# Kernel tuning notes

Hardware: AMD Instinct MI355X
Metric: run time of the kernel (lower is better)

## Reference

```python
import jax, jax.numpy as jnp
import numpy as np

TOP_K = 2  # config.num_experts_per_tok


def quick_gelu(x):
    return x * jax.nn.sigmoid(1.702 * x)


def setup_inputs() -> dict:
    key = jax.random.key(0)
    ks = jax.random.split(key, 6)
    B, S, H, I, E = 8, 4096, 512, 1024, 8
    s_h = 1.0 / np.sqrt(H).astype(np.float32)
    s_i = 1.0 / np.sqrt(I).astype(np.float32)
    return {
        "hidden_states": jax.random.normal(ks[0], (B, S, H), jnp.float32),
        "router_w": jax.random.normal(ks[1], (H, E), jnp.float32) * s_h,
        "router_b": jnp.zeros((E,), jnp.float32),
        "gate_up_proj": jax.random.normal(ks[2], (E, H, 2 * I), jnp.float32) * s_h,
        "gate_up_proj_bias": jnp.zeros((E, 2 * I), jnp.float32),
        "down_proj": jax.random.normal(ks[3], (E, I, H), jnp.float32) * s_i,
        "down_proj_bias": jnp.zeros((E, H), jnp.float32),
    }


def reference(hidden_states, router_w, router_b, gate_up_proj,
              gate_up_proj_bias, down_proj, down_proj_bias):
    B, S, H = hidden_states.shape
    E = router_b.shape[0]
    x = hidden_states.reshape(-1, H)          # [T, H]
    T = x.shape[0]

    # Router: top-k logits then softmax over the selected k
    logits = x @ router_w + router_b          # [T, E]
    top_w, sel = jax.lax.top_k(logits, TOP_K)  # [T, k]
    top_w = jax.nn.softmax(top_w, axis=-1)

    # Per-token per-expert combine weight (0 for unselected experts) [T, E]
    tok_w = jnp.zeros((T, E), x.dtype).at[jnp.arange(T)[:, None], sel].add(top_w)

    # Loop over the (small, fixed) expert axis; zero weights kill non-routed
    # tokens' contributions, matching the masked gather/scatter exactly.
    def body(acc, params):
        Wgu, bgu, Wd, bd, w_e = params        # w_e: [T]
        gu = x @ Wgu + bgu                    # [T, 2I]
        gate, up = jnp.split(gu, 2, axis=-1)
        act = (up + 1.0) * quick_gelu(gate)   # [T, I]
        out = act @ Wd + bd                   # [T, H]
        return acc + out * w_e[:, None], None

    acc0 = jnp.zeros((T, H), x.dtype)
    acc, _ = jax.lax.scan(
        body, acc0,
        (gate_up_proj, gate_up_proj_bias, down_proj, down_proj_bias, tok_w.T))
    return acc.reshape(B, S, H)
```

## Files before the change

### kernel.cpp

```cpp
#include <hip/hip_runtime.h>

#define T_TOK 32768
#define HDIM  512
#define IDIM  1024
#define NEXP  8
#define BM    64
#define KI    128

typedef float    f32x4 __attribute__((ext_vector_type(4)));
typedef _Float16 f16x8 __attribute__((ext_vector_type(8)));
typedef _Float16 f16x4 __attribute__((ext_vector_type(4)));

#define GL2LDS(gp, lp)                                                        \
    __builtin_amdgcn_global_load_lds(                                         \
        (const __attribute__((address_space(1))) void*)(gp),                  \
        (__attribute__((address_space(3))) void*)(lp), 16, 0, 0)

__global__ __launch_bounds__(256) void router_kernel(
    const float* __restrict__ x, const float* __restrict__ rw,
    const float* __restrict__ rb, int* __restrict__ cnt,
    int* __restrict__ btok, float* __restrict__ bw)
{
    __shared__ float Wl[HDIM * NEXP];
    __shared__ float xc[64 * 133];
    __shared__ float part[4 * 64 * 8];
    __shared__ int   bcnt[NEXP];
    __shared__ int   sbase[NEXP];

    const int tid = threadIdx.x;
    const int t0  = blockIdx.x * 64;

    if (tid < NEXP) bcnt[tid] = 0;

    for (int j = tid; j < HDIM * NEXP / 4; j += 256)
        ((float4*)Wl)[j] = ((const float4*)rw)[j];

    const int tl = tid & 63;
    const int q  = tid >> 6;

    float acc[8];
#pragma unroll
    for (int e = 0; e < 8; ++e) acc[e] = 0.f;

    for (int hc = 0; hc < 4; ++hc) {
        __syncthreads();
        for (int j = tid; j < 64 * 128 / 4; j += 256) {
            int row = j >> 5;
            int col = (j & 31) * 4;
            float4 v = *(const float4*)(x + (size_t)(t0 + row) * HDIM + hc * 128 + col);
            float* d = &xc[row * 133 + col];
            d[0] = v.x; d[1] = v.y; d[2] = v.z; d[3] = v.w;
        }
        __syncthreads();
#pragma unroll
        for (int hh = 0; hh < 32; ++hh) {
            int h = q * 32 + hh;
            float xv = xc[tl * 133 + h];
            const float* wrow = &Wl[(hc * 128 + h) * 8];
#pragma unroll
            for (int e = 0; e < 8; ++e) acc[e] += xv * wrow[e];
        }
    }
#pragma unroll
    for (int e = 0; e < 8; ++e) part[(q * 64 + tl) * 8 + e] = acc[e];
    __syncthreads();

    int e0 = 0, e1 = 0, l0 = 0, l1 = 0;
    float w0 = 0.f, w1 = 0.f;
    if (tid < 64) {
        float lg[8];
#pragma unroll
        for (int e = 0; e < 8; ++e)
            lg[e] = part[(0 * 64 + tid) * 8 + e] + part[(1 * 64 + tid) * 8 + e] +
                    part[(2 * 64 + tid) * 8 + e] + part[(3 * 64 + tid) * 8 + e] + rb[e];
#pragma unroll
        for (int e = 1; e < 8; ++e) if (lg[e] > lg[e0]) e0 = e;
        e1 = (e0 == 0) ? 1 : 0;
#pragma unroll
        for (int e = 0; e < 8; ++e) if (e != e0 && lg[e] > lg[e1]) e1 = e;
        float z = __expf(lg[e1] - lg[e0]);
        w0 = 1.f / (1.f + z);
        w1 = z * w0;
        l0 = atomicAdd(&bcnt[e0], 1);
        l1 = atomicAdd(&bcnt[e1], 1);
    }
    __syncthreads();
    if (tid < NEXP) sbase[tid] = atomicAdd(&cnt[tid], bcnt[tid]);
    __syncthreads();
    if (tid < 64) {
        int t  = t0 + tid;
        int s0 = sbase[e0] + l0;
        btok[e0 * T_TOK + s0] = t;  bw[e0 * T_TOK + s0] = w0;
        int s1 = sbase[e1] + l1;
        btok[e1 * T_TOK + s1] = t;  bw[e1 * T_TOK + s1] = w1;
    }
}

template <int R, int C>
__global__ __launch_bounds__(256) void transpose_cvt(
    const float* __restrict__ src, _Float16* __restrict__ dst)
{
    __shared__ float tile[32][33];
    const int e  = blockIdx.z;
    const int rb = blockIdx.y * 32, cb = blockIdx.x * 32;
    const int t  = threadIdx.x;
    {
        const int lr = t >> 3, lc = (t & 7) * 4;
        float4 v = *(const float4*)(src + ((size_t)e * R + rb + lr) * C + cb + lc);
        tile[lr][lc + 0] = v.x; tile[lr][lc + 1] = v.y;
        tile[lr][lc + 2] = v.z; tile[lr][lc + 3] = v.w;
    }
    __syncthreads();
    {
        const int c = t >> 3, r4 = (t & 7) * 4;
        f16x4 h;
        h[0] = (_Float16)tile[r4 + 0][c];
        h[1] = (_Float16)tile[r4 + 1][c];
        h[2] = (_Float16)tile[r4 + 2][c];
        h[3] = (_Float16)tile[r4 + 3][c];
        *(f16x4*)(dst + ((size_t)e * C + cb + c) * R + rb + r4) = h;
    }
}

__global__ __launch_bounds__(512) void moe_kernel(
    const float* __restrict__ x,
    const _Float16* __restrict__ wgu_t,
    const float* __restrict__ bgu,
    const _Float16* __restrict__ wd_t,
    const float* __restrict__ bd,
    const int* __restrict__ cnt,
    const int* __restrict__ btok,
    const float* __restrict__ bw,
    float* __restrict__ out)
{
    const int bid = blockIdx.x;
    const int e   = bid & 7;
    const int m0  = (bid >> 3) * BM;
    const int n_e = cnt[e];
    if (m0 >= n_e) return;

    __shared__ __align__(16) _Float16 A[BM * HDIM];
    __shared__ __align__(16) _Float16 BGU[2 * 8192];
    __shared__ __align__(16) _Float16 ACT[2][BM * KI];
    __shared__ int   s_tok[BM];
    __shared__ float s_w[BM];

    const int tid  = threadIdx.x;
    const int lane = tid & 63;
    const int wv   = tid >> 6;
    const int bn   = lane & 15;
    const int bk   = (lane >> 4) * 8;

    const int d1 = tid * 16;
    const int u1 = d1 ^ (((d1 >> 7) & 7) << 4);
    const int d2 = d1 + 8192;
    const int u2 = d2 ^ (((d2 >> 7) & 7) << 4);
    const _Float16* wguE = wgu_t + (size_t)e * 2 * IDIM * HDIM;
    const _Float16* sp1  = wguE + ((size_t)(((u1 >> 6) & 1) * IDIM + (u1 >> 7))) * HDIM + ((u1 & 63) >> 1);
    const _Float16* sp2  = wguE + ((size_t)(((u2 >> 6) & 1) * IDIM + (u2 >> 7))) * HDIM + ((u2 & 63) >> 1);
    _Float16* lp1 = BGU + tid * 8;
    _Float16* lp2 = lp1 + 4096;

    if (tid < BM) {
        int idx = m0 + tid;
        if (idx < n_e) { s_tok[tid] = btok[e * T_TOK + idx]; s_w[tid] = bw[e * T_TOK + idx]; }
        else           { s_tok[tid] = -1;                    s_w[tid] = 0.f; }
    }
    __syncthreads();

    GL2LDS(sp1, lp1);
    GL2LDS(sp2, lp2);

    {
        const int r  = tid >> 3;
        const int tk = s_tok[r];
#pragma unroll
        for (int j = 0; j < 8; ++j) {
            const int c = ((tid & 7) + j * 8) * 8;
            float4 f0, f1;
            if (tk >= 0) {
                const float4* p = (const float4*)(x + (size_t)tk * HDIM + c);
                f0 = p[0]; f1 = p[1];
            } else { f0 = make_float4(0, 0, 0, 0); f1 = f0; }
            f16x8 h;
            h[0] = (_Float16)f0.x; h[1] = (_Float16)f0.y;
            h[2] = (_Float16)f0.z; h[3] = (_Float16)f0.w;
            h[4] = (_Float16)f1.x; h[5] = (_Float16)f1.y;
            h[6] = (_Float16)f1.z; h[7] = (_Float16)f1.w;
            int byte = r * 1024 + c * 2;  byte ^= (r & 7) << 4;
            *(f16x8*)((char*)A + byte) = h;
        }
    }

    f32x4 accO[4][4];
#pragma unroll
    for (int mt = 0; mt < 4; ++mt)
#pragma unroll
        for (int nt = 0; nt < 4; ++nt)
#pragma unroll
            for (int r = 0; r < 4; ++r) accO[mt][nt][r] = 0.f;

    const int colu = wv * 16 + bn;
    const int sw   = (colu & 7) << 4;
    const int bgOff = colu * 128 + ((bk * 2) ^ sw);
    const int buOff = colu * 128 + ((64 + bk * 2) ^ sw);

    for (int ic = 0; ic < IDIM / KI; ++ic) {
        f32x4 accG[4], accU[4];
#pragma unroll
        for (int mt = 0; mt < 4; ++mt)
#pragma unroll
            for (int r = 0; r < 4; ++r) { accG[mt][r] = 0.f; accU[mt][r] = 0.f; }

        for (int ks = 0; ks < 16; ++ks) {
            __syncthreads();
            if (ks < 15) {
                const _Float16* q1 = sp1 + (size_t)ic * KI * HDIM + (ks + 1) * 32;
                const _Float16* q2 = sp2 + (size_t)ic * KI * HDIM + (ks + 1) * 32;
                _Float16* t1 = lp1 + ((ks + 1) & 1) * 8192;
                _Float16* t2 = lp2 + ((ks + 1) & 1) * 8192;
                GL2LDS(q1, t1);
                GL2LDS(q2, t2);
            } else if (ic < IDIM / KI - 1) {
                const _Float16* q1 = sp1 + (size_t)(ic + 1) * KI * HDIM;
                const _Float16* q2 = sp2 + (size_t)(ic + 1) * KI * HDIM;
                GL2LDS(q1, lp1);
                GL2LDS(q2, lp2);
            }

            const char* bb = (const char*)BGU + (ks & 1) * 16384;
            f16x8 bgf = *(const f16x8*)(bb + bgOff);
            f16x8 buf_ = *(const f16x8*)(bb + buOff);
            const int k0b = (ks * 32 + bk) * 2;
#pragma unroll
            for (int mt = 0; mt < 4; ++mt) {
                const int m = mt * 16 + bn;
                int byte = m * 1024 + k0b;  byte ^= (m & 7) << 4;
                f16x8 af = *(const f16x8*)((const char*)A + byte);
                accG[mt] = __builtin_amdgcn_mfma_f32_16x16x32_f16(af, bgf, accG[mt], 0, 0, 0);
                accU[mt] = __builtin_amdgcn_mfma_f32_16x16x32_f16(af, buf_, accU[mt], 0, 0, 0);
            }
        }

        char* actb = (char*)ACT + (ic & 1) * (BM * KI * 2);
        const int   gidx = e * 2 * IDIM + ic * KI + colu;
        const float bgv  = bgu[gidx];
        const float buv  = bgu[gidx + IDIM];
#pragma unroll
        for (int mt = 0; mt < 4; ++mt) {
#pragma unroll
            for (int r = 0; r < 4; ++r) {
                float g = accG[mt][r] + bgv;
                float u = accU[mt][r] + buv;
                float a = (u + 1.f) * g / (1.f + __expf(-1.702f * g));
                const int row = mt * 16 + ((lane >> 4) << 2) + r;
                int byte = row * 256 + colu * 2;  byte ^= (row & 7) << 4;
                *(_Float16*)(actb + byte) = (_Float16)a;
            }
        }
        __syncthreads();

        const _Float16* bdp = wd_t + ((size_t)(e * HDIM) + wv * 64) * IDIM;
#pragma unroll
        for (int ks = 0; ks < 4; ++ks) {
            const int kl = ks * 32 + bk;
            const int kg = ic * KI + kl;
            f16x8 bf[4];
#pragma unroll
            for (int nt = 0; nt < 4; ++nt)
                bf[nt] = *(const f16x8*)(bdp + (size_t)(nt * 16 + bn) * IDIM + kg);
#pragma unroll
            for (int mt = 0; mt < 4; ++mt) {
                const int m = mt * 16 + bn;
                int byte = m * 256 + kl * 2;  byte ^= (m & 7) << 4;
                f16x8 af = *(const f16x8*)((const char*)actb + byte);
#pragma unroll
                for (int nt = 0; nt < 4; ++nt)
                    accO[mt][nt] = __builtin_amdgcn_mfma_f32_16x16x32_f16(af, bf[nt], accO[mt][nt], 0, 0, 0);
            }
        }
    }

    float bdv[4];
#pragma unroll
    for (int nt = 0; nt < 4; ++nt) bdv[nt] = bd[e * HDIM + wv * 64 + nt * 16 + bn];
#pragma unroll
    for (int mt = 0; mt < 4; ++mt) {
#pragma unroll
        for (int r = 0; r < 4; ++r) {
            const int m  = mt * 16 + ((lane >> 4) << 2) + r;
            const int tk = s_tok[m];
            if (tk < 0) continue;
            const float wgt = s_w[m];
            float* orow = out + (size_t)tk * HDIM + wv * 64 + bn;
#pragma unroll
            for (int nt = 0; nt < 4; ++nt)
                atomicAdd(orow + nt * 16, (accO[mt][nt][r] + bdv[nt]) * wgt);
        }
    }
}

extern "C" void kernel_launch(void* const* d_in, const int* in_sizes, int n_in,
                              void* d_out, int out_size, void* d_ws, size_t ws_size,
                              hipStream_t stream)
{
    const float* x   = (const float*)d_in[0];
    const float* rw  = (const float*)d_in[1];
    const float* rb  = (const float*)d_in[2];
    const float* wgu = (const float*)d_in[3];
    const float* bgu = (const float*)d_in[4];
    const float* wd  = (const float*)d_in[5];
    const float* bd  = (const float*)d_in[6];
    float* out = (float*)d_out;

    char* ws = (char*)d_ws;
    size_t o = 0;
    int*   cnt  = (int*)(ws + o);   o += 256;
    int*   btok = (int*)(ws + o);   o += (size_t)NEXP * T_TOK * 4;
    float* bwp  = (float*)(ws + o); o += (size_t)NEXP * T_TOK * 4;
    _Float16* wgu_t = (_Float16*)(ws + o); o += (size_t)NEXP * 2 * IDIM * HDIM * 2;
    _Float16* wd_t  = (_Float16*)(ws + o); o += (size_t)NEXP * HDIM * IDIM * 2;

    hipMemsetAsync(cnt, 0, 256, stream);
    hipMemsetAsync(out, 0, (size_t)out_size * 4, stream);

    transpose_cvt<HDIM, 2 * IDIM><<<dim3(2 * IDIM / 32, HDIM / 32, NEXP), 256, 0, stream>>>(wgu, wgu_t);
    transpose_cvt<IDIM, HDIM><<<dim3(HDIM / 32, IDIM / 32, NEXP), 256, 0, stream>>>(wd, wd_t);
    router_kernel<<<T_TOK / 64, 256, 0, stream>>>(x, rw, rb, cnt, btok, bwp);
    moe_kernel<<<dim3((T_TOK / BM) * NEXP), 512, 0, stream>>>(
        x, wgu_t, bgu, wd_t, bd, cnt, btok, bwp, out);
}
```

Before: 748.2 us.

## Deepen gate/up weight prefetch to four LDS stages with vmcnt-based barriers

Grows the gate/up weight LDS ring from two to four stages, so async global-to-LDS loads run three k-steps ahead instead of one. Full __syncthreads are replaced by an explicit partial vmcnt wait plus s_barrier, so each step blocks only on the oldest stage rather than on every outstanding load. It also raises wave priority around the MFMA blocks, batches the activation reads for the down projection, and hoists the bias loads. The ACT buffer drops to a single copy to make room, which brings LDS use close to the per-workgroup limit.

Result: faster. 687.4 us (-8.1%).

```diff
diff --git a/kernel.cpp b/kernel.cpp
--- a/kernel.cpp
+++ b/kernel.cpp
@@ -15,6 +15,12 @@
     __builtin_amdgcn_global_load_lds(                                         \
         (const __attribute__((address_space(1))) void*)(gp),                  \
         (__attribute__((address_space(3))) void*)(lp), 16, 0, 0)
+
+#define LGKM_BAR()                                                            \
+    do {                                                                      \
+        asm volatile("s_waitcnt lgkmcnt(0)" ::: "memory");                    \
+        __builtin_amdgcn_s_barrier();                                         \
+    } while (0)
 
 __global__ __launch_bounds__(256) void router_kernel(
     const float* __restrict__ x, const float* __restrict__ rw,
@@ -140,8 +146,8 @@
     if (m0 >= n_e) return;
 
     __shared__ __align__(16) _Float16 A[BM * HDIM];
-    __shared__ __align__(16) _Float16 BGU[2 * 8192];
-    __shared__ __align__(16) _Float16 ACT[2][BM * KI];
+    __shared__ __align__(16) _Float16 BGU[4 * 8192];
+    __shared__ __align__(16) _Float16 ACT[BM * KI];
     __shared__ int   s_tok[BM];
     __shared__ float s_w[BM];
 
@@ -158,18 +164,21 @@
     const _Float16* wguE = wgu_t + (size_t)e * 2 * IDIM * HDIM;
     const _Float16* sp1  = wguE + ((size_t)(((u1 >> 6) & 1) * IDIM + (u1 >> 7))) * HDIM + ((u1 & 63) >> 1);
     const _Float16* sp2  = wguE + ((size_t)(((u2 >> 6) & 1) * IDIM + (u2 >> 7))) * HDIM + ((u2 & 63) >> 1);
-    _Float16* lp1 = BGU + tid * 8;
-    _Float16* lp2 = lp1 + 4096;
 
     if (tid < BM) {
         int idx = m0 + tid;
         if (idx < n_e) { s_tok[tid] = btok[e * T_TOK + idx]; s_w[tid] = bw[e * T_TOK + idx]; }
         else           { s_tok[tid] = -1;                    s_w[tid] = 0.f; }
     }
-    __syncthreads();
-
-    GL2LDS(sp1, lp1);
-    GL2LDS(sp2, lp2);
+    LGKM_BAR();
+
+#pragma unroll
+    for (int s = 0; s < 3; ++s) {
+        const size_t off = (size_t)(s & 15) * 32;
+        _Float16* t1 = BGU + s * 8192 + tid * 8;
+        GL2LDS(sp1 + off, t1);
+        GL2LDS(sp2 + off, t1 + 4096);
+    }
 
     {
         const int r  = tid >> 3;
@@ -191,6 +200,7 @@
             *(f16x8*)((char*)A + byte) = h;
         }
     }
+    LGKM_BAR();
 
     f32x4 accO[4][4];
 #pragma unroll
@@ -206,32 +216,34 @@
     const int buOff = colu * 128 + ((64 + bk * 2) ^ sw);
 
     for (int ic = 0; ic < IDIM / KI; ++ic) {
+        const int   gidx = e * 2 * IDIM + ic * KI + colu;
+        const float bgv  = bgu[gidx];
+        const float buv  = bgu[gidx + IDIM];
+
         f32x4 accG[4], accU[4];
 #pragma unroll
         for (int mt = 0; mt < 4; ++mt)
 #pragma unroll
             for (int r = 0; r < 4; ++r) { accG[mt][r] = 0.f; accU[mt][r] = 0.f; }
 
+#pragma unroll
         for (int ks = 0; ks < 16; ++ks) {
-            __syncthreads();
-            if (ks < 15) {
-                const _Float16* q1 = sp1 + (size_t)ic * KI * HDIM + (ks + 1) * 32;
-                const _Float16* q2 = sp2 + (size_t)ic * KI * HDIM + (ks + 1) * 32;
-                _Float16* t1 = lp1 + ((ks + 1) & 1) * 8192;
-                _Float16* t2 = lp2 + ((ks + 1) & 1) * 8192;
-                GL2LDS(q1, t1);
-                GL2LDS(q2, t2);
-            } else if (ic < IDIM / KI - 1) {
-                const _Float16* q1 = sp1 + (size_t)(ic + 1) * KI * HDIM;
-                const _Float16* q2 = sp2 + (size_t)(ic + 1) * KI * HDIM;
-                GL2LDS(q1, lp1);
-                GL2LDS(q2, lp2);
+            asm volatile("s_waitcnt vmcnt(4)" ::: "memory");
+            __builtin_amdgcn_s_barrier();
+
+            const int s3 = ic * 16 + ks + 3;
+            if (s3 < (IDIM / KI) * 16) {
+                const size_t off = (size_t)(s3 >> 4) * KI * HDIM + (size_t)(s3 & 15) * 32;
+                _Float16* t1 = BGU + ((ks + 3) & 3) * 8192 + tid * 8;
+                GL2LDS(sp1 + off, t1);
+                GL2LDS(sp2 + off, t1 + 4096);
             }
 
-            const char* bb = (const char*)BGU + (ks & 1) * 16384;
-            f16x8 bgf = *(const f16x8*)(bb + bgOff);
+            const char* bb = (const char*)BGU + (ks & 3) * 16384;
+            f16x8 bgf  = *(const f16x8*)(bb + bgOff);
             f16x8 buf_ = *(const f16x8*)(bb + buOff);
             const int k0b = (ks * 32 + bk) * 2;
+            __builtin_amdgcn_s_setprio(1);
 #pragma unroll
             for (int mt = 0; mt < 4; ++mt) {
                 const int m = mt * 16 + bn;
@@ -240,12 +252,9 @@
                 accG[mt] = __builtin_amdgcn_mfma_f32_16x16x32_f16(af, bgf, accG[mt], 0, 0, 0);
                 accU[mt] = __builtin_amdgcn_mfma_f32_16x16x32_f16(af, buf_, accU[mt], 0, 0, 0);
             }
-        }
-
-        char* actb = (char*)ACT + (ic & 1) * (BM * KI * 2);
-        const int   gidx = e * 2 * IDIM + ic * KI + colu;
-        const float bgv  = bgu[gidx];
-        const float buv  = bgu[gidx + IDIM];
+            __builtin_amdgcn_s_setprio(0);
+        }
+
 #pragma unroll
         for (int mt = 0; mt < 4; ++mt) {
 #pragma unroll
@@ -255,10 +264,10 @@
                 float a = (u + 1.f) * g / (1.f + __expf(-1.702f * g));
                 const int row = mt * 16 + ((lane >> 4) << 2) + r;
                 int byte = row * 256 + colu * 2;  byte ^= (row & 7) << 4;
-                *(_Float16*)(actb + byte) = (_Float16)a;
+                *(_Float16*)((char*)ACT + byte) = (_Float16)a;
             }
         }
-        __syncthreads();
+        LGKM_BAR();
 
         const _Float16* bdp = wd_t + ((size_t)(e * HDIM) + wv * 64) * IDIM;
 #pragma unroll
@@ -269,15 +278,21 @@
 #pragma unroll
             for (int nt = 0; nt < 4; ++nt)
                 bf[nt] = *(const f16x8*)(bdp + (size_t)(nt * 16 + bn) * IDIM + kg);
+            f16x8 af2[4];
 #pragma unroll
             for (int mt = 0; mt < 4; ++mt) {
                 const int m = mt * 16 + bn;
                 int byte = m * 256 + kl * 2;  byte ^= (m & 7) << 4;
-                f16x8 af = *(const f16x8*)((const char*)actb + byte);
+                af2[mt] = *(const f16x8*)((const char*)ACT + byte);
+            }
+            __builtin_amdgcn_s_setprio(1);
+#pragma unroll
+            for (int mt = 0; mt < 4; ++mt)
 #pragma unroll
                 for (int nt = 0; nt < 4; ++nt)
-                    accO[mt][nt] = __builtin_amdgcn_mfma_f32_16x16x32_f16(af, bf[nt], accO[mt][nt], 0, 0, 0);
-            }
+                    accO[mt][nt] = __builtin_amdgcn_mfma_f32_16x16x32_f16(
+                        af2[mt], bf[nt], accO[mt][nt], 0, 0, 0);
+            __builtin_amdgcn_s_setprio(0);
         }
     }
 
```
